# Kernel tuning notes

Measured on AMD Instinct MI355X. Metric: run time of the kernel, lower is better.

## Reference

```python
import jax, jax.numpy as jnp
import numpy as np

B, S, H, NH = 2, 2048, 1024, 16
HD = H // NH  # head dim = 64


def setup_inputs() -> dict:
    key = jax.random.key(0)
    k_in, k_q, k_kv, k_o = jax.random.split(key, 4)
    scale = 0.02
    return {
        "inputs": jax.random.normal(k_in, (B, S, H), dtype=jnp.float32),
        "Wq": jax.random.normal(k_q, (H, H), dtype=jnp.float32) * scale,
        "bq": jnp.zeros((H,), dtype=jnp.float32),
        "Wkv": jax.random.normal(k_kv, (H, 2 * H), dtype=jnp.float32) * scale,
        "bkv": jnp.zeros((2 * H,), dtype=jnp.float32),
        "Wo": jax.random.normal(k_o, (H, H), dtype=jnp.float32) * scale,
        "bo": jnp.zeros((H,), dtype=jnp.float32),
    }


def reference(inputs, Wq, bq, Wkv, bkv, Wo, bo):
    b, s, h = inputs.shape
    q = inputs @ Wq + bq                      # [B,S,H]
    kv = inputs @ Wkv + bkv                   # [B,S,2H]
    k, v = kv[..., :h], kv[..., h:]           # each [B,S,H]
    q = q.reshape(b, s, NH, HD)
    k = k.reshape(b, s, NH, HD)
    v = v.reshape(b, s, NH, HD)
    inv_sqrt_d = jnp.asarray(1.0 / np.sqrt(HD), dtype=inputs.dtype)
    scores = jnp.einsum("bqhd,bkhd->bhqk", q, k) * inv_sqrt_d  # [B,NH,S,S]
    probs = jax.nn.softmax(scores, axis=-1)
    attended = jnp.einsum("bhqk,bkhd->bqhd", probs, v)         # [B,S,NH,HD]
    attended = attended.reshape(b, s, h)
    return attended @ Wo + bo
```

## Files before the change

kernel.cpp:

```cpp
#include <hip/hip_runtime.h>
#include <cstdint>

typedef __bf16 bf16;
typedef __attribute__((ext_vector_type(8))) __bf16 bf16x8;
typedef __attribute__((ext_vector_type(4))) __bf16 bf16v4;
typedef __attribute__((ext_vector_type(4))) float f32x4;
typedef __attribute__((ext_vector_type(16))) float f32x16;

#define MFMA16(a, b, c) __builtin_amdgcn_mfma_f32_16x16x32_bf16((a), (b), (c), 0, 0, 0)
#define MFMA32(a, b, c) __builtin_amdgcn_mfma_f32_32x32x16_bf16((a), (b), (c), 0, 0, 0)

#define BATCH 2
#define SLEN 2048
#define HDIM 1024
#define NHEAD 16
#define HEADD 64
#define MROWS (BATCH * SLEN)

#define CEXP 0.1803368801f

typedef __attribute__((address_space(3))) void lds_void;
typedef const __attribute__((address_space(1))) void glb_void;
__device__ __forceinline__ void load_lds16(const bf16* g, bf16* l) {
    __builtin_amdgcn_global_load_lds((glb_void*)g, (lds_void*)l, 16, 0, 0);
}

__global__ __launch_bounds__(256) void prep_kernel(const float* __restrict__ X,
                                                   const float* __restrict__ Wq,
                                                   const float* __restrict__ Wkv,
                                                   const float* __restrict__ Wo,
                                                   const float* __restrict__ bq,
                                                   const float* __restrict__ bkv,
                                                   bf16* __restrict__ Xbf,
                                                   bf16* __restrict__ WqkvT,
                                                   bf16* __restrict__ WoT,
                                                   float* __restrict__ bqkv) {
    const int blk = blockIdx.x;
    const int tid = threadIdx.x;
    if (blk < 4096) {
        int i = (blk * 256 + tid) * 4;
        float4 v = *(const float4*)&X[i];
        bf16v4 o;
        o[0] = (bf16)v.x; o[1] = (bf16)v.y; o[2] = (bf16)v.z; o[3] = (bf16)v.w;
        *(bf16v4*)&Xbf[i] = o;
        return;
    }
    if (blk < 8192) {
        const float* in; bf16* out; int C, id;
        if (blk < 5120)      { in = Wq;  out = WqkvT;                C = 1024; id = blk - 4096; }
        else if (blk < 7168) { in = Wkv; out = WqkvT + 1024 * 1024;  C = 2048; id = blk - 5120; }
        else                 { in = Wo;  out = WoT;                  C = 1024; id = blk - 7168; }
        const int R = 1024;
        const int nbx = C / 32;
        const int j0 = (id % nbx) * 32, i0 = (id / nbx) * 32;
        const int tx = tid & 31, ty = tid >> 5;
        __shared__ float t[32][33];
        for (int r = ty; r < 32; r += 8)
            t[r][tx] = in[(size_t)(i0 + r) * C + j0 + tx];
        __syncthreads();
        for (int r = ty; r < 32; r += 8)
            out[(size_t)(j0 + r) * R + i0 + tx] = (bf16)t[tx][r];
        return;
    }
    int i = (blk - 8192) * 256 + tid;
    if (i < 3072) bqkv[i] = (i < 1024) ? bq[i] : bkv[i - 1024];
}

template <int BM, int BN, int EPI>
__global__ __launch_bounds__(256) void gemm2_kernel(const bf16* __restrict__ A,
                                                    const bf16* __restrict__ BT,
                                                    const float* __restrict__ bias,
                                                    bf16* __restrict__ oQ,
                                                    bf16* __restrict__ oK,
                                                    bf16* __restrict__ oVT,
                                                    float* __restrict__ oF, int K) {
    constexpr int WM = BM / 2, WN = BN / 2;
    constexpr int MT = WM / 16, NT = WN / 16;

    const int tid = threadIdx.x;
    const int lane = tid & 63, wid = tid >> 6;
    const int l15 = lane & 15, quad = lane >> 4;
    const int wm = (wid >> 1) * WM, wn = (wid & 1) * WN;
    const int m0 = blockIdx.y * BM, n0 = blockIdx.x * BN;

    __shared__ bf16 As[BM * 32];
    __shared__ bf16 Bs[BN * 32];

    f32x4 acc[MT][NT] = {};

    const bf16* Ag = A + (size_t)m0 * K;
    const bf16* Bg = BT + (size_t)n0 * K;
    const int arow = lane >> 2, acol = (lane & 3) * 8;

    for (int k0 = 0; k0 < K; k0 += 32) {
#pragma unroll
        for (int t = 0; t < BM / 64; ++t) {
            int tt = t * 4 + wid;
            load_lds16(Ag + (size_t)(tt * 16 + arow) * K + k0 + acol, &As[tt * 512]);
        }
#pragma unroll
        for (int t = 0; t < BN / 64; ++t) {
            int tt = t * 4 + wid;
            load_lds16(Bg + (size_t)(tt * 16 + arow) * K + k0 + acol, &Bs[tt * 512]);
        }
        __syncthreads();

        bf16x8 af[MT], bfr[NT];
#pragma unroll
        for (int i = 0; i < MT; ++i)
            af[i] = *(const bf16x8*)&As[(wm + i * 16 + l15) * 32 + quad * 8];
#pragma unroll
        for (int j = 0; j < NT; ++j)
            bfr[j] = *(const bf16x8*)&Bs[(wn + j * 16 + l15) * 32 + quad * 8];
#pragma unroll
        for (int i = 0; i < MT; ++i)
#pragma unroll
            for (int j = 0; j < NT; ++j)
                acc[i][j] = MFMA16(af[i], bfr[j], acc[i][j]);
        __syncthreads();
    }

#pragma unroll
    for (int i = 0; i < MT; ++i) {
#pragma unroll
        for (int j = 0; j < NT; ++j) {
            const int mb = m0 + wm + i * 16 + quad * 4;
            const int n = n0 + wn + j * 16 + l15;
            const float bv = bias[n];
            if (EPI == 2) {
                float* o = oF + (size_t)mb * 1024 + n;
#pragma unroll
                for (int r = 0; r < 4; ++r) o[(size_t)r * 1024] = acc[i][j][r] + bv;
            } else if (n0 < 1024) {
#pragma unroll
                for (int r = 0; r < 4; ++r)
                    oQ[(size_t)(mb + r) * 1024 + n] = (bf16)((acc[i][j][r] + bv) * CEXP);
            } else if (n0 < 2048) {
#pragma unroll
                for (int r = 0; r < 4; ++r)
                    oK[(size_t)(mb + r) * 1024 + (n - 1024)] = (bf16)(acc[i][j][r] + bv);
            } else {
                const int hd = n - 2048;
                const int bb = mb >> 11, ss = mb & 2047;
                bf16v4 pk;
#pragma unroll
                for (int r = 0; r < 4; ++r) pk[r] = (bf16)(acc[i][j][r] + bv);
                *(bf16v4*)&oVT[((size_t)(bb << 10) + hd) * 2048 + ss] = pk;
            }
        }
    }
}

__global__ __launch_bounds__(256) void attn5_kernel(const bf16* __restrict__ Q,
                                                    const bf16* __restrict__ K,
                                                    const bf16* __restrict__ VT,
                                                    bf16* __restrict__ O) {
    const int bh = blockIdx.y;
    const int b = bh >> 4, head = bh & 15;
    const int q0 = blockIdx.x * 128;
    const int tid = threadIdx.x;
    const int lane = tid & 63, wid = tid >> 6;
    const int l31 = lane & 31, hh = lane >> 5;

    __shared__ bf16 Ks[64 * 64];
    __shared__ bf16 VTs[64 * 64];
    __shared__ bf16 Ps[4][32 * 72];

    const int qw = q0 + wid * 32;
    bf16x8 qf[4];
#pragma unroll
    for (int kd = 0; kd < 4; ++kd)
        qf[kd] = *(const bf16x8*)&Q[(size_t)(b * SLEN + qw + l31) * HDIM +
                                    head * 64 + kd * 16 + hh * 8];

    f32x16 o_acc[2] = {};
    float l_lane = 0.f;

    const bf16* Kg = K + (size_t)b * SLEN * HDIM + head * 64;
    const bf16* Vg = VT + (size_t)bh * 64 * SLEN;

    const int srow = lane >> 3, slot = lane & 7;
    const int schunk = slot ^ srow;

    for (int kt = 0; kt < 32; ++kt) {
        const int k0 = kt * 64;
        {
            const int rbase = wid * 16;
#pragma unroll
            for (int pass = 0; pass < 2; ++pass) {
                const int rb = rbase + pass * 8;
                load_lds16(Kg + (size_t)(k0 + rb + srow) * HDIM + schunk * 8, &Ks[rb * 64]);
                load_lds16(Vg + (size_t)(rb + srow) * SLEN + k0 + schunk * 8, &VTs[rb * 64]);
            }
        }
        __syncthreads();

        f32x16 sacc[2] = {};
#pragma unroll
        for (int kd = 0; kd < 4; ++kd)
#pragma unroll
            for (int mt = 0; mt < 2; ++mt) {
                const int row = mt * 32 + l31;
                const int c = (kd * 2 + hh) ^ (row & 7);
                bf16x8 kf = *(const bf16x8*)&Ks[row * 64 + c * 8];
                sacc[mt] = MFMA32(kf, qf[kd], sacc[mt]);
            }

#pragma unroll
        for (int mt = 0; mt < 2; ++mt)
#pragma unroll
            for (int g = 0; g < 4; ++g) {
                bf16v4 pk;
#pragma unroll
                for (int r = 0; r < 4; ++r) {
                    float p = __builtin_amdgcn_exp2f(sacc[mt][g * 4 + r]);
                    l_lane += p;
                    pk[r] = (bf16)p;
                }
                *(bf16v4*)&Ps[wid][l31 * 72 + mt * 32 + g * 8 + 4 * hh] = pk;
            }

#pragma unroll
        for (int kstep = 0; kstep < 4; ++kstep) {
            bf16x8 pf = *(const bf16x8*)&Ps[wid][l31 * 72 + kstep * 16 + hh * 8];
#pragma unroll
            for (int mt = 0; mt < 2; ++mt) {
                const int row = mt * 32 + l31;
                const int c = (kstep * 2 + hh) ^ (row & 7);
                bf16x8 vf = *(const bf16x8*)&VTs[row * 64 + c * 8];
                o_acc[mt] = MFMA32(vf, pf, o_acc[mt]);
            }
        }
        __syncthreads();
    }

    const float l_full = l_lane + __shfl_xor(l_lane, 32, 64);
    const float inv = 1.f / l_full;
    bf16* orow = O + (size_t)(b * SLEN + qw + l31) * HDIM + head * 64;
#pragma unroll
    for (int mt = 0; mt < 2; ++mt)
#pragma unroll
        for (int g = 0; g < 4; ++g) {
            bf16v4 pk;
#pragma unroll
            for (int r = 0; r < 4; ++r) pk[r] = (bf16)(o_acc[mt][g * 4 + r] * inv);
            *(bf16v4*)&orow[mt * 32 + g * 8 + 4 * hh] = pk;
        }
}

extern "C" void kernel_launch(void* const* d_in, const int* in_sizes, int n_in,
                              void* d_out, int out_size, void* d_ws, size_t ws_size,
                              hipStream_t stream) {
    const float* X   = (const float*)d_in[0];
    const float* Wq  = (const float*)d_in[1];
    const float* bq  = (const float*)d_in[2];
    const float* Wkv = (const float*)d_in[3];
    const float* bkv = (const float*)d_in[4];
    const float* Wo  = (const float*)d_in[5];
    const float* bo  = (const float*)d_in[6];
    float* out = (float*)d_out;

    char* ws = (char*)d_ws;
    bf16* Xbf   = (bf16*)(ws);
    bf16* WqkvT = (bf16*)(ws + (8ull << 20));
    bf16* WoT   = (bf16*)(ws + (14ull << 20));
    float* bqkv = (float*)(ws + (16ull << 20));
    bf16* Qbf   = (bf16*)(ws + (17ull << 20));
    bf16* Kbf   = (bf16*)(ws + (25ull << 20));
    bf16* VTbf  = (bf16*)(ws + (33ull << 20));
    bf16* Abf   = (bf16*)(ws + (41ull << 20));

    prep_kernel<<<8204, 256, 0, stream>>>(X, Wq, Wkv, Wo, bq, bkv, Xbf, WqkvT, WoT, bqkv);

    gemm2_kernel<128, 128, 1><<<dim3(3072 / 128, MROWS / 128), 256, 0, stream>>>(
        Xbf, WqkvT, bqkv, Qbf, Kbf, VTbf, nullptr, 1024);

    attn5_kernel<<<dim3(SLEN / 128, BATCH * NHEAD), 256, 0, stream>>>(Qbf, Kbf, VTbf, Abf);

    gemm2_kernel<128, 64, 2><<<dim3(1024 / 64, MROWS / 128), 256, 0, stream>>>(
        Abf, WoT, bo, nullptr, nullptr, nullptr, out, 1024);
}
```

Before: 204.6 us.

## Double attention key tile to 128 and remap blocks so each XCD shares heads

The attention kernel now stages 128 keys of K and V^T per iteration instead of 64, halving the number of barrier pairs and loop iterations, with the XOR swizzle widened to 16 chunks for the wider V^T rows. The grid is flattened to 1D and block IDs are remapped so that all 16 query tiles of a given batch-head land on the same XCD, improving L2 reuse of K/V. The larger LDS footprint may reduce occupancy.

```diff
diff --git a/kernel.cpp b/kernel.cpp
--- a/kernel.cpp
+++ b/kernel.cpp
@@ -151,19 +151,21 @@
     }
 }
 
-__global__ __launch_bounds__(256) void attn5_kernel(const bf16* __restrict__ Q,
+__global__ __launch_bounds__(256) void attn6_kernel(const bf16* __restrict__ Q,
                                                     const bf16* __restrict__ K,
                                                     const bf16* __restrict__ VT,
                                                     bf16* __restrict__ O) {
-    const int bh = blockIdx.y;
+    const int bid = blockIdx.x;
+    const int xcd = bid & 7, j = bid >> 3;
+    const int bh = xcd * 4 + (j >> 4);
+    const int q0 = (j & 15) * 128;
     const int b = bh >> 4, head = bh & 15;
-    const int q0 = blockIdx.x * 128;
     const int tid = threadIdx.x;
     const int lane = tid & 63, wid = tid >> 6;
     const int l31 = lane & 31, hh = lane >> 5;
 
-    __shared__ bf16 Ks[64 * 64];
-    __shared__ bf16 VTs[64 * 64];
+    __shared__ bf16 Ks[128 * 64];
+    __shared__ bf16 VTs[64 * 128];
     __shared__ bf16 Ps[4][32 * 72];
 
     const int qw = q0 + wid * 32;
@@ -179,56 +181,59 @@
     const bf16* Kg = K + (size_t)b * SLEN * HDIM + head * 64;
     const bf16* Vg = VT + (size_t)bh * 64 * SLEN;
 
-    const int srow = lane >> 3, slot = lane & 7;
-    const int schunk = slot ^ srow;
-
-    for (int kt = 0; kt < 32; ++kt) {
-        const int k0 = kt * 64;
-        {
-            const int rbase = wid * 16;
-#pragma unroll
-            for (int pass = 0; pass < 2; ++pass) {
-                const int rb = rbase + pass * 8;
-                load_lds16(Kg + (size_t)(k0 + rb + srow) * HDIM + schunk * 8, &Ks[rb * 64]);
-                load_lds16(Vg + (size_t)(rb + srow) * SLEN + k0 + schunk * 8, &VTs[rb * 64]);
-            }
-        }
-        __syncthreads();
-
-        f32x16 sacc[2] = {};
-#pragma unroll
-        for (int kd = 0; kd < 4; ++kd)
-#pragma unroll
-            for (int mt = 0; mt < 2; ++mt) {
-                const int row = mt * 32 + l31;
-                const int c = (kd * 2 + hh) ^ (row & 7);
-                bf16x8 kf = *(const bf16x8*)&Ks[row * 64 + c * 8];
-                sacc[mt] = MFMA32(kf, qf[kd], sacc[mt]);
-            }
-
-#pragma unroll
-        for (int mt = 0; mt < 2; ++mt)
-#pragma unroll
-            for (int g = 0; g < 4; ++g) {
-                bf16v4 pk;
-#pragma unroll
-                for (int r = 0; r < 4; ++r) {
-                    float p = __builtin_amdgcn_exp2f(sacc[mt][g * 4 + r]);
-                    l_lane += p;
-                    pk[r] = (bf16)p;
+    const int r8 = lane >> 3, p8 = lane & 7;
+    const int r16 = lane >> 4, p16 = lane & 15;
+
+    for (int kt = 0; kt < 16; ++kt) {
+        const int k0 = kt * 128;
+#pragma unroll
+        for (int pass = 0; pass < 4; ++pass) {
+            const int rbk = pass * 32 + wid * 8;
+            load_lds16(Kg + (size_t)(k0 + rbk + r8) * HDIM + ((p8 ^ ((rbk + r8) & 7)) * 8),
+                       &Ks[rbk * 64]);
+            const int rbv = pass * 16 + wid * 4;
+            load_lds16(Vg + (size_t)(rbv + r16) * SLEN + k0 + ((p16 ^ ((rbv + r16) & 15)) * 8),
+                       &VTs[rbv * 128]);
+        }
+        __syncthreads();
+
+#pragma unroll
+        for (int h = 0; h < 2; ++h) {
+            f32x16 sacc[2] = {};
+#pragma unroll
+            for (int kd = 0; kd < 4; ++kd)
+#pragma unroll
+                for (int m = 0; m < 2; ++m) {
+                    const int key = (h * 2 + m) * 32 + l31;
+                    const int c = (kd * 2 + hh) ^ (key & 7);
+                    bf16x8 kf = *(const bf16x8*)&Ks[key * 64 + c * 8];
+                    sacc[m] = MFMA32(kf, qf[kd], sacc[m]);
                 }
-                *(bf16v4*)&Ps[wid][l31 * 72 + mt * 32 + g * 8 + 4 * hh] = pk;
-            }
-
-#pragma unroll
-        for (int kstep = 0; kstep < 4; ++kstep) {
-            bf16x8 pf = *(const bf16x8*)&Ps[wid][l31 * 72 + kstep * 16 + hh * 8];
-#pragma unroll
-            for (int mt = 0; mt < 2; ++mt) {
-                const int row = mt * 32 + l31;
-                const int c = (kstep * 2 + hh) ^ (row & 7);
-                bf16x8 vf = *(const bf16x8*)&VTs[row * 64 + c * 8];
-                o_acc[mt] = MFMA32(vf, pf, o_acc[mt]);
+
+#pragma unroll
+            for (int m = 0; m < 2; ++m)
+#pragma unroll
+                for (int g = 0; g < 4; ++g) {
+                    bf16v4 pk;
+#pragma unroll
+                    for (int r = 0; r < 4; ++r) {
+                        float p = __builtin_amdgcn_exp2f(sacc[m][g * 4 + r]);
+                        l_lane += p;
+                        pk[r] = (bf16)p;
+                    }
+                    *(bf16v4*)&Ps[wid][l31 * 72 + m * 32 + g * 8 + 4 * hh] = pk;
+                }
+
+#pragma unroll
+            for (int kstep = 0; kstep < 4; ++kstep) {
+                bf16x8 pf = *(const bf16x8*)&Ps[wid][l31 * 72 + kstep * 16 + hh * 8];
+#pragma unroll
+                for (int dt = 0; dt < 2; ++dt) {
+                    const int d = dt * 32 + l31;
+                    const int cc = ((h * 4 + kstep) * 2 + hh) ^ (d & 15);
+                    bf16x8 vf = *(const bf16x8*)&VTs[d * 128 + cc * 8];
+                    o_acc[dt] = MFMA32(vf, pf, o_acc[dt]);
+                }
             }
         }
         __syncthreads();
@@ -275,7 +280,7 @@
     gemm2_kernel<128, 128, 1><<<dim3(3072 / 128, MROWS / 128), 256, 0, stream>>>(
         Xbf, WqkvT, bqkv, Qbf, Kbf, VTbf, nullptr, 1024);
 
-    attn5_kernel<<<dim3(SLEN / 128, BATCH * NHEAD), 256, 0, stream>>>(Qbf, Kbf, VTbf, Abf);
+    attn6_kernel<<<512, 256, 0, stream>>>(Qbf, Kbf, VTbf, Abf);
 
     gemm2_kernel<128, 64, 2><<<dim3(1024 / 64, MROWS / 128), 256, 0, stream>>>(
         Abf, WoT, bo, nullptr, nullptr, nullptr, out, 1024);
```

New measurement: 198.2 us. -3.1%, faster.
